# Optimization experiments

Measured on AMD Instinct MI355X. Metric: run time of the kernel, lower is better.

Reference implementation:

```python
import jax, jax.numpy as jnp
import numpy as np

E = 1024   # d_model
H = 16     # nhead
DH = E // H
F = 4096   # dim_feedforward
B, S = 4, 1024
EPS = 1e-5


def setup_inputs() -> dict:
    key = jax.random.key(0)
    ks = jax.random.split(key, 12)
    s = 0.02
    return {
        "src": jax.random.normal(ks[0], (B, S, E), jnp.float32),
        "src_mask": jnp.zeros((S, S), jnp.float32),
        "w_qkv": jax.random.normal(ks[1], (3 * E, E), jnp.float32) * s,
        "b_qkv": jnp.zeros((3 * E,), jnp.float32),
        "w_o": jax.random.normal(ks[2], (E, E), jnp.float32) * s,
        "b_o": jnp.zeros((E,), jnp.float32),
        "w1": jax.random.normal(ks[3], (F, E), jnp.float32) * s,
        "b1": jnp.zeros((F,), jnp.float32),
        "w2": jax.random.normal(ks[4], (E, F), jnp.float32) * s,
        "b2": jnp.zeros((E,), jnp.float32),
        "ln1_g": jnp.ones((E,), jnp.float32),
        "ln1_b": jnp.zeros((E,), jnp.float32),
        "ln2_g": jnp.ones((E,), jnp.float32),
        "ln2_b": jnp.zeros((E,), jnp.float32),
    }


def _layer_norm(x, g, b):
    mu = jnp.mean(x, axis=-1, keepdims=True)
    var = jnp.mean(jnp.square(x - mu), axis=-1, keepdims=True)
    return (x - mu) * jax.lax.rsqrt(var + EPS) * g + b


def reference(src, src_mask, w_qkv, b_qkv, w_o, b_o, w1, b1, w2, b2,
              ln1_g, ln1_b, ln2_g, ln2_b):
    # dropout in eval mode (identity). Math matches nn.MultiheadAttention
    # with need_weights=True, average_attn_weights=False.
    b, s, e = src.shape
    qkv = src @ w_qkv.T + b_qkv                      # [B,S,3E]
    q, k, v = jnp.split(qkv, 3, axis=-1)
    q = q.reshape(b, s, H, DH)
    k = k.reshape(b, s, H, DH)
    v = v.reshape(b, s, H, DH)
    scale = 1.0 / np.sqrt(DH)
    scores = jnp.einsum('bqhd,bkhd->bhqk', q, k) * scale + src_mask  # [B,H,S,S]
    attn_weights = jax.nn.softmax(scores, axis=-1)                   # [B,H,S,S]
    ctx = jnp.einsum('bhqk,bkhd->bqhd', attn_weights, v).reshape(b, s, e)
    attn_out = ctx @ w_o.T + b_o
    x = _layer_norm(src + attn_out, ln1_g, ln1_b)
    ffn = jax.nn.relu(x @ w1.T + b1) @ w2.T + b2
    x = _layer_norm(x + ffn, ln2_g, ln2_b)
    return x, attn_weights
```

## Files before the change

kernel.cpp:

```cpp
#include <hip/hip_runtime.h>
#include <cstdint>

typedef __bf16 bf16;
typedef bf16 bf16x8 __attribute__((ext_vector_type(8)));
typedef bf16 bf16x4 __attribute__((ext_vector_type(4)));
typedef float f32x4 __attribute__((ext_vector_type(4)));
typedef uint32_t u32;

static constexpr int E_ = 1024;
static constexpr int H_ = 16;
static constexpr int DH_ = 64;
static constexpr int F_ = 4096;
static constexpr int B_ = 4;
static constexpr int S_ = 1024;
static constexpr long TOK = (long)B_ * S_;

__device__ static __forceinline__ void gld16(const void* g, void* l) {
  __builtin_amdgcn_global_load_lds(
      (const __attribute__((address_space(1))) u32*)g,
      (__attribute__((address_space(3))) u32*)l, 16, 0, 0);
}

__device__ __forceinline__ f32x4 mfma16(bf16x8 a, bf16x8 b, f32x4 c) {
  return __builtin_amdgcn_mfma_f32_16x16x32_bf16(a, b, c, 0, 0, 0);
}

__global__ __launch_bounds__(256) void f2b_all(
    const float* __restrict__ s0, bf16* __restrict__ d0,
    const float* __restrict__ s1, bf16* __restrict__ d1,
    const float* __restrict__ s2, bf16* __restrict__ d2,
    const float* __restrict__ s3, bf16* __restrict__ d3,
    const float* __restrict__ s4, bf16* __restrict__ d4) {
  long v = (long)blockIdx.x * 256 + threadIdx.x;
  const float* in;
  bf16* out;
  long off;
  if (v < 524288)        { in = s0; out = d0; off = v; }
  else if (v < 917504)   { in = s1; out = d1; off = v - 524288; }
  else if (v < 1048576)  { in = s2; out = d2; off = v - 917504; }
  else if (v < 1572864)  { in = s3; out = d3; off = v - 1048576; }
  else                   { in = s4; out = d4; off = v - 1572864; }
  const float4* p = (const float4*)in + off * 2;
  float4 a = p[0], b = p[1];
  bf16x8 o = {(bf16)a.x, (bf16)a.y, (bf16)a.z, (bf16)a.w,
              (bf16)b.x, (bf16)b.y, (bf16)b.z, (bf16)b.w};
  *((bf16x8*)out + off) = o;
}

enum { EPI_BIAS_F32 = 0, EPI_BIAS_RELU_BF16 = 1, EPI_QKV = 2, EPI_BIAS_RES_F32 = 3 };

template <int EPI, int BN>
__global__ __launch_bounds__(256, 2) void gemm_nt(
    const bf16* __restrict__ A, const bf16* __restrict__ Bm,
    float* __restrict__ Cf, bf16* __restrict__ Cb,
    bf16* __restrict__ Qh, bf16* __restrict__ Kh, bf16* __restrict__ Vt,
    const float* __restrict__ bias, const float* __restrict__ res,
    int K, int ldc) {
  constexpr int NJ = BN / 32;
  __shared__ bf16 Sm[128 * 64 + BN * 64];
  bf16* As = Sm;
  bf16* Bs = Sm + 128 * 64;
  const int tid = threadIdx.x, lane = tid & 63, wave = tid >> 6;
  const int quad = lane >> 4, l16 = lane & 15;
  const int wm = wave >> 1, wn = wave & 1;
  const int row0 = blockIdx.y * 128, col0 = blockIdx.x * BN;

  const long ldab = (long)K * 2;
  const char* Ag = (const char*)A +
                   (long)(row0 + wave * 32 + (lane >> 3)) * ldab + (lane & 7) * 16;
  const char* Bg = (const char*)Bm +
                   (long)(col0 + wave * (BN / 4) + (lane >> 3)) * ldab + (lane & 7) * 16;
  char* Al = (char*)As + (wave * 32 + (lane >> 3)) * 128 + (lane & 7) * 16;
  char* Bl = (char*)Bs + (wave * (BN / 4) + (lane >> 3)) * 128 + (lane & 7) * 16;

  f32x4 acc[4][NJ];
#pragma unroll
  for (int i = 0; i < 4; i++)
#pragma unroll
    for (int j = 0; j < NJ; j++) acc[i][j] = (f32x4){0.f, 0.f, 0.f, 0.f};

  for (int k0 = 0; k0 < K; k0 += 64) {
    __syncthreads();
#pragma unroll
    for (int c = 0; c < 4; c++) gld16(Ag + (long)c * 8 * ldab + k0 * 2, Al + c * 1024);
#pragma unroll
    for (int c = 0; c < BN / 32; c++) gld16(Bg + (long)c * 8 * ldab + k0 * 2, Bl + c * 1024);
    __syncthreads();
#pragma unroll
    for (int kk = 0; kk < 2; kk++) {
      bf16x8 af[4], bfr[NJ];
#pragma unroll
      for (int i = 0; i < 4; i++)
        af[i] = *(const bf16x8*)&As[(wm * 64 + i * 16 + l16) * 64 + kk * 32 + quad * 8];
#pragma unroll
      for (int j = 0; j < NJ; j++)
        bfr[j] = *(const bf16x8*)&Bs[(wn * (BN / 2) + j * 16 + l16) * 64 + kk * 32 + quad * 8];
#pragma unroll
      for (int i = 0; i < 4; i++)
#pragma unroll
        for (int j = 0; j < NJ; j++) acc[i][j] = mfma16(af[i], bfr[j], acc[i][j]);
    }
  }

  if constexpr (EPI == EPI_QKV) {
    const int which = col0 >> 10;
    if (which == 2) {
      bf16* T = Sm;
      __syncthreads();
#pragma unroll
      for (int i = 0; i < 4; i++)
#pragma unroll
        for (int j = 0; j < NJ; j++)
#pragma unroll
          for (int r = 0; r < 4; r++) {
            int row_l = wm * 64 + i * 16 + quad * 4 + r;
            int col_l = wn * 64 + j * 16 + l16;
            float t = acc[i][j][r] + bias[col0 + col_l];
            T[col_l * 128 + (row_l ^ ((col_l & 7) << 4))] = (bf16)t;
          }
      __syncthreads();
      const int b_ = row0 >> 10;
      const int s0 = row0 & 1023;
#pragma unroll
      for (int g = 0; g < 8; g++) {
        int col_l = wave * 32 + g * 4 + quad;
        int nn = (col0 + col_l) & 1023;
        int h_ = nn >> 6, d_ = nn & 63;
        int sl = l16 * 8;
        bf16x8 vv = *(const bf16x8*)&T[col_l * 128 + (sl ^ ((col_l & 7) << 4))];
        *(bf16x8*)&Vt[(((long)(b_ * H_ + h_)) * DH_ + d_) * S_ + s0 + sl] = vv;
      }
    } else {
#pragma unroll
      for (int i = 0; i < 4; i++)
#pragma unroll
        for (int j = 0; j < NJ; j++)
#pragma unroll
          for (int r = 0; r < 4; r++) {
            int row = row0 + wm * 64 + i * 16 + quad * 4 + r;
            int col = col0 + wn * (BN / 2) + j * 16 + l16;
            float t = acc[i][j][r] + bias[col];
            int b_ = row >> 10, s_ = row & 1023;
            int nn = col & 1023;
            int h_ = nn >> 6, d_ = nn & 63;
            long q = (((long)(b_ * H_ + h_)) * S_ + s_) * DH_ + d_;
            if (which == 0) Qh[q] = (bf16)t;
            else Kh[q] = (bf16)t;
          }
    }
  } else {
#pragma unroll
    for (int i = 0; i < 4; i++)
#pragma unroll
      for (int j = 0; j < NJ; j++)
#pragma unroll
        for (int r = 0; r < 4; r++) {
          int row = row0 + wm * 64 + i * 16 + quad * 4 + r;
          int col = col0 + wn * (BN / 2) + j * 16 + l16;
          float v = acc[i][j][r];
          if constexpr (EPI == EPI_BIAS_F32) {
            Cf[(long)row * ldc + col] = v + bias[col];
          } else if constexpr (EPI == EPI_BIAS_RES_F32) {
            Cf[(long)row * ldc + col] = v + bias[col] + res[(long)row * ldc + col];
          } else {
            Cb[(long)row * ldc + col] = (bf16)fmaxf(v + bias[col], 0.f);
          }
        }
  }
}

__global__ __launch_bounds__(256, 2) void attn_pass1(
    const bf16* __restrict__ Q, const bf16* __restrict__ K,
    const float* __restrict__ mask, float* __restrict__ rowsum) {
  __shared__ bf16 Qs[128 * 64];
  __shared__ bf16 Ks[128 * 64];
  const int tid = threadIdx.x, lane = tid & 63, wave = tid >> 6;
  const int quad = lane >> 4, l16 = lane & 15;
  const int q0 = blockIdx.x * 128, bh = blockIdx.y;
  const bf16* Qb = Q + ((long)bh * S_ + q0) * DH_;
  const bf16* Kb = K + (long)bh * S_ * DH_;

  {
    const char* g = (const char*)Qb + wave * 4096 + lane * 16;
    char* l = (char*)Qs + wave * 4096 + lane * 16;
#pragma unroll
    for (int c = 0; c < 4; c++) gld16(g + c * 1024, l + c * 1024);
  }

  float rs[2][4];
#pragma unroll
  for (int i = 0; i < 2; i++)
#pragma unroll
    for (int r = 0; r < 4; r++) rs[i][r] = 0.f;

  for (int t = 0; t < 8; t++) {
    __syncthreads();
    {
      const char* g = (const char*)Kb + (long)t * 16384 + wave * 4096 + lane * 16;
      char* l = (char*)Ks + wave * 4096 + lane * 16;
#pragma unroll
      for (int c = 0; c < 4; c++) gld16(g + c * 1024, l + c * 1024);
    }
    __syncthreads();
    f32x4 acc[2][8];
#pragma unroll
    for (int i = 0; i < 2; i++)
#pragma unroll
      for (int j = 0; j < 8; j++) acc[i][j] = (f32x4){0.f, 0.f, 0.f, 0.f};
#pragma unroll
    for (int kk = 0; kk < 2; kk++) {
      bf16x8 af[2], bfr[8];
#pragma unroll
      for (int i = 0; i < 2; i++)
        af[i] = *(const bf16x8*)&Qs[(wave * 32 + i * 16 + l16) * 64 + kk * 32 + quad * 8];
#pragma unroll
      for (int j = 0; j < 8; j++)
        bfr[j] = *(const bf16x8*)&Ks[(j * 16 + l16) * 64 + kk * 32 + quad * 8];
#pragma unroll
      for (int i = 0; i < 2; i++)
#pragma unroll
        for (int j = 0; j < 8; j++) acc[i][j] = mfma16(af[i], bfr[j], acc[i][j]);
    }
#pragma unroll
    for (int i = 0; i < 2; i++)
#pragma unroll
      for (int j = 0; j < 8; j++)
#pragma unroll
        for (int r = 0; r < 4; r++) {
          int qr = q0 + wave * 32 + i * 16 + quad * 4 + r;
          int gcol = t * 128 + j * 16 + l16;
          float sv = acc[i][j][r] * 0.125f + mask[(long)qr * S_ + gcol];
          rs[i][r] += __expf(sv);
        }
  }
#pragma unroll
  for (int i = 0; i < 2; i++)
#pragma unroll
    for (int r = 0; r < 4; r++) {
      float v = rs[i][r];
      v += __shfl_xor(v, 1);
      v += __shfl_xor(v, 2);
      v += __shfl_xor(v, 4);
      v += __shfl_xor(v, 8);
      if (l16 == 0)
        rowsum[(long)bh * S_ + q0 + wave * 32 + i * 16 + quad * 4 + r] = v;
    }
}

__global__ __launch_bounds__(256, 2) void attn_pass2(
    const bf16* __restrict__ Q, const bf16* __restrict__ K,
    const bf16* __restrict__ V, const float* __restrict__ mask,
    const float* __restrict__ rowsum, float* __restrict__ W,
    bf16* __restrict__ ctxb) {
  __shared__ bf16 Qs[128 * 64];
  __shared__ bf16 Ks[128 * 64];
  __shared__ bf16 Ps[128 * 136];
  const int tid = threadIdx.x, lane = tid & 63, wave = tid >> 6;
  const int quad = lane >> 4, l16 = lane & 15;
  const int q0 = blockIdx.x * 128, bh = blockIdx.y;
  const bf16* Qb = Q + ((long)bh * S_ + q0) * DH_;
  const bf16* Kb = K + (long)bh * S_ * DH_;
  const bf16* Vb = V + (long)bh * DH_ * S_;

  float rinv[2][4];
#pragma unroll
  for (int i = 0; i < 2; i++)
#pragma unroll
    for (int r = 0; r < 4; r++)
      rinv[i][r] =
          1.0f / rowsum[(long)bh * S_ + q0 + wave * 32 + i * 16 + quad * 4 + r];

  {
    const char* g = (const char*)Qb + wave * 4096 + lane * 16;
    char* l = (char*)Qs + wave * 4096 + lane * 16;
#pragma unroll
    for (int c = 0; c < 4; c++) gld16(g + c * 1024, l + c * 1024);
  }

  f32x4 cacc[2][4];
#pragma unroll
  for (int i = 0; i < 2; i++)
#pragma unroll
    for (int j = 0; j < 4; j++) cacc[i][j] = (f32x4){0.f, 0.f, 0.f, 0.f};

  for (int t = 0; t < 8; t++) {
    __syncthreads();
    {
      const char* g = (const char*)Kb + (long)t * 16384 + wave * 4096 + lane * 16;
      char* l = (char*)Ks + wave * 4096 + lane * 16;
#pragma unroll
      for (int c = 0; c < 4; c++) gld16(g + c * 1024, l + c * 1024);
    }
    __syncthreads();
    f32x4 acc[2][8];
#pragma unroll
    for (int i = 0; i < 2; i++)
#pragma unroll
      for (int j = 0; j < 8; j++) acc[i][j] = (f32x4){0.f, 0.f, 0.f, 0.f};
#pragma unroll
    for (int kk = 0; kk < 2; kk++) {
      bf16x8 af[2], bfr[8];
#pragma unroll
      for (int i = 0; i < 2; i++)
        af[i] = *(const bf16x8*)&Qs[(wave * 32 + i * 16 + l16) * 64 + kk * 32 + quad * 8];
#pragma unroll
      for (int j = 0; j < 8; j++)
        bfr[j] = *(const bf16x8*)&Ks[(j * 16 + l16) * 64 + kk * 32 + quad * 8];
#pragma unroll
      for (int i = 0; i < 2; i++)
#pragma unroll
        for (int j = 0; j < 8; j++) acc[i][j] = mfma16(af[i], bfr[j], acc[i][j]);
    }
#pragma unroll
    for (int i = 0; i < 2; i++)
#pragma unroll
      for (int j = 0; j < 8; j++)
#pragma unroll
        for (int r = 0; r < 4; r++) {
          int ql = wave * 32 + i * 16 + quad * 4 + r;
          int qr = q0 + ql;
          int col = j * 16 + l16, gcol = t * 128 + col;
          float u = __expf(acc[i][j][r] * 0.125f + mask[(long)qr * S_ + gcol]) *
                    rinv[i][r];
          __builtin_nontemporal_store(u, &W[((long)bh * S_ + qr) * S_ + gcol]);
          Ps[ql * 136 + col] = (bf16)u;
        }
    __syncthreads();
#pragma unroll
    for (int kk = 0; kk < 4; kk++) {
      bf16x8 pf[2], vf[4];
#pragma unroll
      for (int i = 0; i < 2; i++)
        pf[i] = *(const bf16x8*)&Ps[(wave * 32 + i * 16 + l16) * 136 + kk * 32 + quad * 8];
#pragma unroll
      for (int j = 0; j < 4; j++)
        vf[j] = *(const bf16x8*)(Vb + (long)(j * 16 + l16) * S_ + t * 128 +
                                 kk * 32 + quad * 8);
#pragma unroll
      for (int i = 0; i < 2; i++)
#pragma unroll
        for (int j = 0; j < 4; j++) cacc[i][j] = mfma16(pf[i], vf[j], cacc[i][j]);
    }
  }
  const int b_ = bh >> 4, h_ = bh & 15;
#pragma unroll
  for (int i = 0; i < 2; i++)
#pragma unroll
    for (int j = 0; j < 4; j++)
#pragma unroll
      for (int r = 0; r < 4; r++) {
        int qr = q0 + wave * 32 + i * 16 + quad * 4 + r;
        ctxb[((long)b_ * S_ + qr) * E_ + h_ * 64 + j * 16 + l16] =
            (bf16)cacc[i][j][r];
      }
}

__global__ __launch_bounds__(256) void ln_kernel(
    const float* __restrict__ a, const float* __restrict__ g,
    const float* __restrict__ beta, float* __restrict__ outf,
    bf16* __restrict__ outb) {
  const int tid = threadIdx.x;
  const int wave = tid >> 6, lane = tid & 63;
  long base = (long)blockIdx.x * E_ + tid * 4;
  float4 x = *(const float4*)(a + base);
  float s = x.x + x.y + x.z + x.w;
  float sq = x.x * x.x + x.y * x.y + x.z * x.z + x.w * x.w;
#pragma unroll
  for (int o = 32; o; o >>= 1) { s += __shfl_xor(s, o); sq += __shfl_xor(sq, o); }
  __shared__ float rs[4], rq[4];
  if (!lane) { rs[wave] = s; rq[wave] = sq; }
  __syncthreads();
  s = rs[0] + rs[1] + rs[2] + rs[3];
  sq = rq[0] + rq[1] + rq[2] + rq[3];
  float mu = s * (1.f / E_);
  float var = sq * (1.f / E_) - mu * mu;
  float rstd = rsqrtf(var + 1e-5f);
  int c = tid * 4;
  float4 gg = *(const float4*)(g + c);
  float4 bb = *(const float4*)(beta + c);
  float o0 = (x.x - mu) * rstd * gg.x + bb.x;
  float o1 = (x.y - mu) * rstd * gg.y + bb.y;
  float o2 = (x.z - mu) * rstd * gg.z + bb.z;
  float o3 = (x.w - mu) * rstd * gg.w + bb.w;
  if (outf) *(float4*)(outf + base) = make_float4(o0, o1, o2, o3);
  if (outb) {
    bf16x4 ob = {(bf16)o0, (bf16)o1, (bf16)o2, (bf16)o3};
    *(bf16x4*)(outb + base) = ob;
  }
}

extern "C" void kernel_launch(void* const* d_in, const int* in_sizes, int n_in,
                              void* d_out, int out_size, void* d_ws, size_t ws_size,
                              hipStream_t stream) {
  const float* src   = (const float*)d_in[0];
  const float* mask  = (const float*)d_in[1];
  const float* w_qkv = (const float*)d_in[2];
  const float* b_qkv = (const float*)d_in[3];
  const float* w_o   = (const float*)d_in[4];
  const float* b_o   = (const float*)d_in[5];
  const float* w1    = (const float*)d_in[6];
  const float* b1    = (const float*)d_in[7];
  const float* w2    = (const float*)d_in[8];
  const float* b2    = (const float*)d_in[9];
  const float* ln1g  = (const float*)d_in[10];
  const float* ln1b  = (const float*)d_in[11];
  const float* ln2g  = (const float*)d_in[12];
  const float* ln2b  = (const float*)d_in[13];

  float* out = (float*)d_out;
  float* attnW = out + TOK * E_;

  char* w = (char*)d_ws;
  auto alloc = [&](size_t bytes) {
    void* p = w;
    w += (bytes + 255) & ~(size_t)255;
    return p;
  };
  bf16* srcb  = (bf16*)alloc(TOK * E_ * 2);
  bf16* wqkvb = (bf16*)alloc((size_t)3 * E_ * E_ * 2);
  bf16* wob   = (bf16*)alloc((size_t)E_ * E_ * 2);
  bf16* w1b   = (bf16*)alloc((size_t)F_ * E_ * 2);
  bf16* w2b   = (bf16*)alloc((size_t)E_ * F_ * 2);
  bf16* Qh    = (bf16*)alloc((size_t)B_ * H_ * S_ * DH_ * 2);
  bf16* Kh    = (bf16*)alloc((size_t)B_ * H_ * S_ * DH_ * 2);
  bf16* Vt    = (bf16*)alloc((size_t)B_ * H_ * DH_ * S_ * 2);
  bf16* ctxb  = (bf16*)alloc(TOK * E_ * 2);
  float* attn_out = (float*)alloc(TOK * E_ * 4);
  float* x1f  = (float*)alloc(TOK * E_ * 4);
  bf16* x1b   = (bf16*)alloc(TOK * E_ * 2);
  bf16* h1b   = (bf16*)alloc(TOK * (size_t)F_ * 2);
  float* ffn2 = (float*)alloc(TOK * E_ * 4);
  float* rowsum = (float*)alloc((size_t)B_ * H_ * S_ * 4);

  f2b_all<<<8192, 256, 0, stream>>>(src, srcb, w_qkv, wqkvb, w_o, wob,
                                    w1, w1b, w2, w2b);

  gemm_nt<EPI_QKV, 128><<<dim3(3 * E_ / 128, TOK / 128), 256, 0, stream>>>(
      srcb, wqkvb, nullptr, nullptr, Qh, Kh, Vt, b_qkv, nullptr, E_, 0);

  attn_pass1<<<dim3(S_ / 128, B_ * H_), 256, 0, stream>>>(Qh, Kh, mask, rowsum);
  attn_pass2<<<dim3(S_ / 128, B_ * H_), 256, 0, stream>>>(Qh, Kh, Vt, mask,
                                                          rowsum, attnW, ctxb);

  gemm_nt<EPI_BIAS_RES_F32, 64><<<dim3(E_ / 64, TOK / 128), 256, 0, stream>>>(
      ctxb, wob, attn_out, nullptr, nullptr, nullptr, nullptr, b_o, src, E_, E_);

  ln_kernel<<<TOK, 256, 0, stream>>>(attn_out, ln1g, ln1b, x1f, x1b);

  gemm_nt<EPI_BIAS_RELU_BF16, 128><<<dim3(F_ / 128, TOK / 128), 256, 0, stream>>>(
      x1b, w1b, nullptr, h1b, nullptr, nullptr, nullptr, b1, nullptr, E_, F_);

  gemm_nt<EPI_BIAS_RES_F32, 64><<<dim3(E_ / 64, TOK / 128), 256, 0, stream>>>(
      h1b, w2b, ffn2, nullptr, nullptr, nullptr, nullptr, b2, x1f, F_, E_);

  ln_kernel<<<TOK, 256, 0, stream>>>(ffn2, ln2g, ln2b, out, nullptr);
}
```

Before: 614.0 us.

## Add 256x256 double-buffered GEMM kernel for QKV and FFN1 projections

Adds a new 512-thread GEMM kernel with 256x256 output tiles, a double-buffered LDS pipeline using staggered global-to-LDS loads, explicit waitcnt/barrier control, and s_setprio around the MFMA bursts. It replaces the 128-tile GEMM for the QKV and FFN1 projections. The larger tiles give more data reuse per LDS load, and the overlapped prefetch is meant to hide memory latency. In exchange the kernel uses 128 KB of LDS and heavy register pressure, and the QKV grid drops to 192 blocks, which may underfill the GPU's compute units.

```diff
diff --git a/kernel.cpp b/kernel.cpp
--- a/kernel.cpp
+++ b/kernel.cpp
@@ -47,13 +47,173 @@
   *((bf16x8*)out + off) = o;
 }
 
-enum { EPI_BIAS_F32 = 0, EPI_BIAS_RELU_BF16 = 1, EPI_QKV = 2, EPI_BIAS_RES_F32 = 3 };
+enum { G_RELU_BF16 = 0, G_QKV = 1 };
+
+template <int EPI>
+__global__ __launch_bounds__(512, 2) void gemm256(
+    const bf16* __restrict__ A, const bf16* __restrict__ Bm,
+    bf16* __restrict__ Cb, bf16* __restrict__ Qh, bf16* __restrict__ Kh,
+    bf16* __restrict__ Vt, const float* __restrict__ bias, int K, int ldc) {
+  __shared__ bf16 S[65536];
+  bf16* A0 = S;
+  bf16* A1 = S + 16384;
+  bf16* B0 = S + 32768;
+  bf16* B1 = S + 49152;
+  const int tid = threadIdx.x, lane = tid & 63, wave = tid >> 6;
+  const int quad = lane >> 4, l16 = lane & 15;
+  const int wm = wave >> 2, wn = wave & 3;
+  const int row0 = blockIdx.y * 256, col0 = blockIdx.x * 256;
+  const int NT = K >> 6;
+
+  const long ldab = (long)K * 2;
+  const char* Ag = (const char*)A + (long)(row0 + (tid >> 3)) * ldab + (tid & 7) * 16;
+  const char* Bg = (const char*)Bm + (long)(col0 + (tid >> 3)) * ldab + (tid & 7) * 16;
+  char* A0c = (char*)A0 + tid * 16;
+  char* A1c = (char*)A1 + tid * 16;
+  char* B0c = (char*)B0 + tid * 16;
+  char* B1c = (char*)B1 + tid * 16;
+
+  f32x4 acc[8][4];
+#pragma unroll
+  for (int m = 0; m < 8; m++)
+#pragma unroll
+    for (int n = 0; n < 4; n++) acc[m][n] = (f32x4){0.f, 0.f, 0.f, 0.f};
+
+#pragma unroll
+  for (int c = 0; c < 4; c++) gld16(Ag + (long)c * 64 * ldab, A0c + c * 8192);
+#pragma unroll
+  for (int c = 0; c < 4; c++) gld16(Bg + (long)c * 64 * ldab, B0c + c * 8192);
+#pragma unroll
+  for (int c = 0; c < 4; c++) gld16(Ag + (long)c * 64 * ldab + 128, A1c + c * 8192);
+
+  auto tile = [&](int kt, const bf16* Ac, const bf16* Bc, char* AcS, char* BoS,
+                  bool last) {
+    if (last)
+      asm volatile("s_waitcnt vmcnt(0)" ::: "memory");
+    else
+      asm volatile("s_waitcnt vmcnt(4)" ::: "memory");
+    __builtin_amdgcn_s_barrier();
+    if (kt + 1 < NT) {
+#pragma unroll
+      for (int c = 0; c < 4; c++)
+        gld16(Bg + (long)c * 64 * ldab + (long)(kt + 1) * 128, BoS + c * 8192);
+    }
+    bf16x8 af[8][2], bfr[2];
+#pragma unroll
+    for (int m = 0; m < 8; m++)
+#pragma unroll
+      for (int kk = 0; kk < 2; kk++)
+        af[m][kk] = *(const bf16x8*)&Ac[(wm * 128 + m * 16 + l16) * 64 + kk * 32 + quad * 8];
+#pragma unroll
+    for (int kk = 0; kk < 2; kk++)
+      bfr[kk] = *(const bf16x8*)&Bc[(wn * 64 + l16) * 64 + kk * 32 + quad * 8];
+    __builtin_amdgcn_s_setprio(1);
+#pragma unroll
+    for (int m = 0; m < 8; m++)
+#pragma unroll
+      for (int kk = 0; kk < 2; kk++)
+        acc[m][0] = mfma16(af[m][kk], bfr[kk], acc[m][0]);
+    __builtin_amdgcn_s_setprio(0);
+    asm volatile("s_waitcnt lgkmcnt(0)" ::: "memory");
+    __builtin_amdgcn_s_barrier();
+#pragma unroll
+    for (int n = 1; n < 4; n++) {
+      if (n < 3 && kt + 2 < NT) {
+#pragma unroll
+        for (int c = 0; c < 2; c++) {
+          int sw = (n - 1) * 2 + c;
+          gld16(Ag + (long)sw * 64 * ldab + (long)(kt + 2) * 128, AcS + sw * 8192);
+        }
+      }
+#pragma unroll
+      for (int kk = 0; kk < 2; kk++)
+        bfr[kk] = *(const bf16x8*)&Bc[(wn * 64 + n * 16 + l16) * 64 + kk * 32 + quad * 8];
+      __builtin_amdgcn_s_setprio(1);
+#pragma unroll
+      for (int m = 0; m < 8; m++)
+#pragma unroll
+        for (int kk = 0; kk < 2; kk++)
+          acc[m][n] = mfma16(af[m][kk], bfr[kk], acc[m][n]);
+      __builtin_amdgcn_s_setprio(0);
+    }
+  };
+
+  for (int kt = 0; kt < NT; kt += 2) {
+    tile(kt, A0, B0, A0c, B1c, false);
+    tile(kt + 1, A1, B1, A1c, B0c, kt + 2 == NT);
+  }
+
+  if constexpr (EPI == G_RELU_BF16) {
+#pragma unroll
+    for (int m = 0; m < 8; m++)
+#pragma unroll
+      for (int n = 0; n < 4; n++)
+#pragma unroll
+        for (int r = 0; r < 4; r++) {
+          int row = row0 + wm * 128 + m * 16 + quad * 4 + r;
+          int col = col0 + wn * 64 + n * 16 + l16;
+          float v = acc[m][n][r] + bias[col];
+          Cb[(long)row * ldc + col] = (bf16)fmaxf(v, 0.f);
+        }
+  } else {
+    const int which = col0 >> 10;
+    if (which == 2) {
+      asm volatile("s_waitcnt lgkmcnt(0) vmcnt(0)" ::: "memory");
+      __builtin_amdgcn_s_barrier();
+      bf16* T = S;
+#pragma unroll
+      for (int m = 0; m < 8; m++)
+#pragma unroll
+        for (int n = 0; n < 4; n++)
+#pragma unroll
+          for (int r = 0; r < 4; r++) {
+            int row_l = wm * 128 + m * 16 + quad * 4 + r;
+            int col_l = wn * 64 + n * 16 + l16;
+            float t = acc[m][n][r] + bias[col0 + col_l];
+            T[col_l * 256 + (row_l ^ ((col_l & 7) << 4))] = (bf16)t;
+          }
+      __syncthreads();
+      const int b_ = row0 >> 10;
+      const int s0 = row0 & 1023;
+#pragma unroll
+      for (int g = 0; g < 8; g++) {
+        int col_l = wave * 32 + g * 4 + quad;
+        int nn = (col0 + col_l) & 1023;
+        int h_ = nn >> 6, d_ = nn & 63;
+#pragma unroll
+        for (int half = 0; half < 2; half++) {
+          int sl = l16 * 8 + half * 128;
+          bf16x8 vv = *(const bf16x8*)&T[col_l * 256 + (sl ^ ((col_l & 7) << 4))];
+          *(bf16x8*)&Vt[(((long)(b_ * H_ + h_)) * DH_ + d_) * S_ + s0 + sl] = vv;
+        }
+      }
+    } else {
+#pragma unroll
+      for (int m = 0; m < 8; m++)
+#pragma unroll
+        for (int n = 0; n < 4; n++)
+#pragma unroll
+          for (int r = 0; r < 4; r++) {
+            int row = row0 + wm * 128 + m * 16 + quad * 4 + r;
+            int col = col0 + wn * 64 + n * 16 + l16;
+            float t = acc[m][n][r] + bias[col];
+            int b_ = row >> 10, s_ = row & 1023;
+            int nn = col & 1023;
+            int h_ = nn >> 6, d_ = nn & 63;
+            long q = (((long)(b_ * H_ + h_)) * S_ + s_) * DH_ + d_;
+            if (which == 0) Qh[q] = (bf16)t;
+            else Kh[q] = (bf16)t;
+          }
+    }
+  }
+}
+
+enum { EPI_BIAS_RES_F32 = 3 };
 
 template <int EPI, int BN>
 __global__ __launch_bounds__(256, 2) void gemm_nt(
     const bf16* __restrict__ A, const bf16* __restrict__ Bm,
     float* __restrict__ Cf, bf16* __restrict__ Cb,
-    bf16* __restrict__ Qh, bf16* __restrict__ Kh, bf16* __restrict__ Vt,
     const float* __restrict__ bias, const float* __restrict__ res,
     int K, int ldc) {
   constexpr int NJ = BN / 32;
@@ -102,71 +262,21 @@
     }
   }
 
-  if constexpr (EPI == EPI_QKV) {
-    const int which = col0 >> 10;
-    if (which == 2) {
-      bf16* T = Sm;
-      __syncthreads();
-#pragma unroll
-      for (int i = 0; i < 4; i++)
-#pragma unroll
-        for (int j = 0; j < NJ; j++)
-#pragma unroll
-          for (int r = 0; r < 4; r++) {
-            int row_l = wm * 64 + i * 16 + quad * 4 + r;
-            int col_l = wn * 64 + j * 16 + l16;
-            float t = acc[i][j][r] + bias[col0 + col_l];
-            T[col_l * 128 + (row_l ^ ((col_l & 7) << 4))] = (bf16)t;
-          }
-      __syncthreads();
-      const int b_ = row0 >> 10;
-      const int s0 = row0 & 1023;
-#pragma unroll
-      for (int g = 0; g < 8; g++) {
-        int col_l = wave * 32 + g * 4 + quad;
-        int nn = (col0 + col_l) & 1023;
-        int h_ = nn >> 6, d_ = nn & 63;
-        int sl = l16 * 8;
-        bf16x8 vv = *(const bf16x8*)&T[col_l * 128 + (sl ^ ((col_l & 7) << 4))];
-        *(bf16x8*)&Vt[(((long)(b_ * H_ + h_)) * DH_ + d_) * S_ + s0 + sl] = vv;
+#pragma unroll
+  for (int i = 0; i < 4; i++)
+#pragma unroll
+    for (int j = 0; j < NJ; j++)
+#pragma unroll
+      for (int r = 0; r < 4; r++) {
+        int row = row0 + wm * 64 + i * 16 + quad * 4 + r;
+        int col = col0 + wn * (BN / 2) + j * 16 + l16;
+        float v = acc[i][j][r];
+        if constexpr (EPI == EPI_BIAS_RES_F32) {
+          Cf[(long)row * ldc + col] = v + bias[col] + res[(long)row * ldc + col];
+        } else {
+          Cb[(long)row * ldc + col] = (bf16)fmaxf(v + bias[col], 0.f);
+        }
       }
-    } else {
-#pragma unroll
-      for (int i = 0; i < 4; i++)
-#pragma unroll
-        for (int j = 0; j < NJ; j++)
-#pragma unroll
-          for (int r = 0; r < 4; r++) {
-            int row = row0 + wm * 64 + i * 16 + quad * 4 + r;
-            int col = col0 + wn * (BN / 2) + j * 16 + l16;
-            float t = acc[i][j][r] + bias[col];
-            int b_ = row >> 10, s_ = row & 1023;
-            int nn = col & 1023;
-            int h_ = nn >> 6, d_ = nn & 63;
-            long q = (((long)(b_ * H_ + h_)) * S_ + s_) * DH_ + d_;
-            if (which == 0) Qh[q] = (bf16)t;
-            else Kh[q] = (bf16)t;
-          }
-    }
-  } else {
-#pragma unroll
-    for (int i = 0; i < 4; i++)
-#pragma unroll
-      for (int j = 0; j < NJ; j++)
-#pragma unroll
-        for (int r = 0; r < 4; r++) {
-          int row = row0 + wm * 64 + i * 16 + quad * 4 + r;
-          int col = col0 + wn * (BN / 2) + j * 16 + l16;
-          float v = acc[i][j][r];
-          if constexpr (EPI == EPI_BIAS_F32) {
-            Cf[(long)row * ldc + col] = v + bias[col];
-          } else if constexpr (EPI == EPI_BIAS_RES_F32) {
-            Cf[(long)row * ldc + col] = v + bias[col] + res[(long)row * ldc + col];
-          } else {
-            Cb[(long)row * ldc + col] = (bf16)fmaxf(v + bias[col], 0.f);
-          }
-        }
-  }
 }
 
 __global__ __launch_bounds__(256, 2) void attn_pass1(
@@ -435,23 +545,23 @@
   f2b_all<<<8192, 256, 0, stream>>>(src, srcb, w_qkv, wqkvb, w_o, wob,
                                     w1, w1b, w2, w2b);
 
-  gemm_nt<EPI_QKV, 128><<<dim3(3 * E_ / 128, TOK / 128), 256, 0, stream>>>(
-      srcb, wqkvb, nullptr, nullptr, Qh, Kh, Vt, b_qkv, nullptr, E_, 0);
+  gemm256<G_QKV><<<dim3(3 * E_ / 256, TOK / 256), 512, 0, stream>>>(
+      srcb, wqkvb, nullptr, Qh, Kh, Vt, b_qkv, E_, 0);
 
   attn_pass1<<<dim3(S_ / 128, B_ * H_), 256, 0, stream>>>(Qh, Kh, mask, rowsum);
   attn_pass2<<<dim3(S_ / 128, B_ * H_), 256, 0, stream>>>(Qh, Kh, Vt, mask,
                                                           rowsum, attnW, ctxb);
 
   gemm_nt<EPI_BIAS_RES_F32, 64><<<dim3(E_ / 64, TOK / 128), 256, 0, stream>>>(
-      ctxb, wob, attn_out, nullptr, nullptr, nullptr, nullptr, b_o, src, E_, E_);
+      ctxb, wob, attn_out, nullptr, b_o, src, E_, E_);
 
   ln_kernel<<<TOK, 256, 0, stream>>>(attn_out, ln1g, ln1b, x1f, x1b);
 
-  gemm_nt<EPI_BIAS_RELU_BF16, 128><<<dim3(F_ / 128, TOK / 128), 256, 0, stream>>>(
-      x1b, w1b, nullptr, h1b, nullptr, nullptr, nullptr, b1, nullptr, E_, F_);
+  gemm256<G_RELU_BF16><<<dim3(F_ / 256, TOK / 256), 512, 0, stream>>>(
+      x1b, w1b, h1b, nullptr, nullptr, nullptr, b1, E_, F_);
 
   gemm_nt<EPI_BIAS_RES_F32, 64><<<dim3(E_ / 64, TOK / 128), 256, 0, stream>>>(
-      h1b, w2b, ffn2, nullptr, nullptr, nullptr, nullptr, b2, x1f, F_, E_);
+      h1b, w2b, ffn2, nullptr, b2, x1f, F_, E_);
 
   ln_kernel<<<TOK, 256, 0, stream>>>(ffn2, ln2g, ln2b, out, nullptr);
 }
```

Result: no change. 622.6 us (+1.4%).
